# Optimization experiments

Measured on AMD Instinct MI355X. Metric: run time of the kernel, lower is better.

The kernel has to match this reference:

```python
import jax, jax.numpy as jnp
import numpy as np

B, L, D = 2, 2048, 1024
H = 16          # num_heads == num_key_value_heads
FD = 16         # feature_dim (q/k head dim)
HD = D // H     # head_dim = 64 (v head dim)
EPS = 1e-5


def setup_inputs() -> dict:
    key = jax.random.key(0)
    k0, k1, k2, k3, k4 = jax.random.split(key, 5)
    scale = 0.02
    return {
        "hidden_states": jax.random.normal(k0, (B, L, D), jnp.float32),
        "Wq": jax.random.normal(k1, (D, H * FD), jnp.float32) * scale,
        "Wk": jax.random.normal(k2, (D, H * FD), jnp.float32) * scale,
        "Wv": jax.random.normal(k3, (D, H * HD), jnp.float32) * scale,
        "Wo": jax.random.normal(k4, (H * HD, D), jnp.float32) * scale,
    }


def reference(hidden_states, Wq, Wk, Wv, Wo):
    # projections (bias-free), split heads: b l (h d) -> b h l d
    q = (hidden_states @ Wq).reshape(B, L, H, FD).transpose(0, 2, 1, 3)
    k = (hidden_states @ Wk).reshape(B, L, H, FD).transpose(0, 2, 1, 3)
    v = (hidden_states @ Wv).reshape(B, L, H, HD).transpose(0, 2, 1, 3)

    # parallel_rebased: squared-dot-product kernel attention, causal,
    # row-normalized by the kernel sum (use_scale=True, use_normalize=True)
    qk_scale = FD ** -0.5
    s = jnp.einsum('bhqd,bhkd->bhqk', q * qk_scale, k)
    s = s * s  # quadratic feature map: (q.k)^2
    causal = jnp.tril(jnp.ones((L, L), dtype=bool))
    s = jnp.where(causal, s, 0.0)
    z = jnp.sum(s, axis=-1)  # [B,H,L]
    o = jnp.einsum('bhqk,bhkd->bhqd', s, v) / (z[..., None] + EPS)

    # merge heads: b h l d -> b l (h d), output projection
    o = o.transpose(0, 2, 1, 3).reshape(B, L, H * HD)
    return o @ Wo
```

## Files before the change

kernel.cpp:

```cpp
#include <hip/hip_runtime.h>
#include <hip/hip_bf16.h>

#define BB 2
#define LL 2048
#define DD 1024
#define HH 16
#define FD 16
#define HD 64
#define EPS 1e-5f
#define RQKV 1536
#define NFIX 4

typedef __attribute__((ext_vector_type(4))) float f32x4;
typedef __attribute__((ext_vector_type(8))) _Float16 f16x8;
typedef __attribute__((ext_vector_type(4))) _Float16 f16x4;

__global__ __launch_bounds__(256) void cast_hs(
    const float* __restrict__ src, _Float16* __restrict__ dst, int n) {
  int idx = (blockIdx.x * 256 + threadIdx.x) * 16;
  if (idx >= n) return;
#pragma unroll
  for (int half = 0; half < 2; half++) {
    float4 a = *(const float4*)(src + idx + half * 8);
    float4 b = *(const float4*)(src + idx + half * 8 + 4);
    f16x8 p = {(_Float16)a.x, (_Float16)a.y, (_Float16)a.z, (_Float16)a.w,
               (_Float16)b.x, (_Float16)b.y, (_Float16)b.z, (_Float16)b.w};
    *(f16x8*)(dst + idx + half * 8) = p;
  }
}

__global__ __launch_bounds__(256) void transpose_qkv(
    const float* __restrict__ Wq, const float* __restrict__ Wk,
    const float* __restrict__ Wv, _Float16* __restrict__ dst) {
  __shared__ _Float16 s[32][40];
  const int ct = blockIdx.x % 48, kt = blockIdx.x / 48;
  const float* src;
  int n0, ncol, drow;
  if (ct < 8) { src = Wq; n0 = ct * 32; ncol = 256; drow = n0; }
  else if (ct < 16) { src = Wk; n0 = (ct - 8) * 32; ncol = 256; drow = 256 + n0; }
  else { src = Wv; n0 = (ct - 16) * 32; ncol = 1024; drow = 512 + n0; }
  const int k0 = kt * 32;
  const int tid = threadIdx.x;
  {
    int r = tid >> 3, c = (tid & 7) * 4;
    float4 v = *(const float4*)(src + (size_t)(k0 + r) * ncol + n0 + c);
    f16x4 p = {(_Float16)v.x, (_Float16)v.y, (_Float16)v.z, (_Float16)v.w};
    *(f16x4*)&s[r][c] = p;
  }
  __syncthreads();
  {
    int n = tid >> 3, kk = (tid & 7) * 4;
    f16x4 o = {s[kk + 0][n], s[kk + 1][n], s[kk + 2][n], s[kk + 3][n]};
    *(f16x4*)(dst + (size_t)(drow + n) * DD + k0 + kk) = o;
  }
}

__global__ __launch_bounds__(256) void transpose_cast(
    const float* __restrict__ src, _Float16* __restrict__ dst, int K, int N) {
  __shared__ _Float16 s[32][40];
  const int n0 = blockIdx.x * 32, k0 = blockIdx.y * 32;
  const int tid = threadIdx.x;
  {
    int r = tid >> 3, c = (tid & 7) * 4;
    float4 v = *(const float4*)(src + (size_t)(k0 + r) * N + n0 + c);
    f16x4 p = {(_Float16)v.x, (_Float16)v.y, (_Float16)v.z, (_Float16)v.w};
    *(f16x4*)&s[r][c] = p;
  }
  __syncthreads();
  {
    int n = tid >> 3, kk = (tid & 7) * 4;
    f16x4 o = {s[kk + 0][n], s[kk + 1][n], s[kk + 2][n], s[kk + 3][n]};
    *(f16x4*)(dst + (size_t)(n0 + n) * K + k0 + kk) = o;
  }
}

template <typename OutT>
__global__ __launch_bounds__(256) void gemm_f16(
    const _Float16* __restrict__ A, const _Float16* __restrict__ Bt,
    OutT* __restrict__ C, int M, int N, int K) {
  __shared__ __attribute__((aligned(16))) _Float16 sA[128 * 64];
  __shared__ __attribute__((aligned(16))) _Float16 sB[64 * 64];
  const int tid = threadIdx.x;
  const int m0 = blockIdx.y * 128, n0 = blockIdx.x * 64;
  const int w = tid >> 6, lane = tid & 63, quad = lane >> 4, l16 = lane & 15;
  const int wm = (w >> 1) * 64, wn = (w & 1) * 32;

  const int sr = tid >> 1, p = tid & 1;
  const int brow = (tid & 127) >> 1;
  const _Float16* Ag = A + (size_t)(m0 + sr) * K + p * 32;
  const _Float16* Bg = Bt + (size_t)(n0 + brow) * K + p * 32;
  _Float16* sAw = &sA[sr * 64];
  _Float16* sBw = &sB[brow * 64];
  const int aswz = sr & 7, bswz = brow & 7;

  f32x4 acc[4][2];
#pragma unroll
  for (int i = 0; i < 4; i++)
#pragma unroll
    for (int j = 0; j < 2; j++) acc[i][j] = (f32x4){0.f, 0.f, 0.f, 0.f};

  f16x8 ar[4], br[4];
  auto LOAD = [&](int k0) {
#pragma unroll
    for (int i = 0; i < 4; i++) ar[i] = *(const f16x8*)(Ag + k0 + i * 8);
    if (tid < 128) {
#pragma unroll
      for (int i = 0; i < 4; i++) br[i] = *(const f16x8*)(Bg + k0 + i * 8);
    }
  };
  LOAD(0);

  int aoff[4], boff[2];
#pragma unroll
  for (int i = 0; i < 4; i++) {
    int row = wm + i * 16 + l16;
    aoff[i] = row * 64 + ((quad ^ (row & 7)) * 8);
  }
#pragma unroll
  for (int j = 0; j < 2; j++) {
    int row = wn + j * 16 + l16;
    boff[j] = row * 64 + ((quad ^ (row & 7)) * 8);
  }

  for (int k0 = 0; k0 < K; k0 += 64) {
    __syncthreads();
#pragma unroll
    for (int i = 0; i < 4; i++)
      *(f16x8*)(sAw + (((4 * p + i) ^ aswz) * 8)) = ar[i];
    if (tid < 128) {
#pragma unroll
      for (int i = 0; i < 4; i++)
        *(f16x8*)(sBw + (((4 * p + i) ^ bswz) * 8)) = br[i];
    }
    __syncthreads();
    if (k0 + 64 < K) LOAD(k0 + 64);

#pragma unroll
    for (int s = 0; s < 2; s++) {
      f16x8 af[4], bf[2];
#pragma unroll
      for (int i = 0; i < 4; i++) {
        int row = wm + i * 16 + l16;
        int col = ((s * 4 + quad) ^ (row & 7)) * 8;
        af[i] = *(const f16x8*)&sA[row * 64 + col];
      }
#pragma unroll
      for (int j = 0; j < 2; j++) {
        int row = wn + j * 16 + l16;
        int col = ((s * 4 + quad) ^ (row & 7)) * 8;
        bf[j] = *(const f16x8*)&sB[row * 64 + col];
      }
#pragma unroll
      for (int i = 0; i < 4; i++)
#pragma unroll
        for (int j = 0; j < 2; j++)
          acc[i][j] = __builtin_amdgcn_mfma_f32_16x16x32_f16(af[i], bf[j], acc[i][j], 0, 0, 0);
    }
  }
  (void)aoff; (void)boff;

#pragma unroll
  for (int i = 0; i < 4; i++)
#pragma unroll
    for (int j = 0; j < 2; j++)
#pragma unroll
      for (int r = 0; r < 4; r++) {
        const int row = m0 + wm + i * 16 + quad * 4 + r;
        const int col = n0 + wn + j * 16 + l16;
        C[(size_t)row * N + col] = (OutT)acc[i][j][r];
      }
}

#define SK4 24
#define SV4 88
#define SS4 88

__global__ __launch_bounds__(256) void attn_mfma4(
    const _Float16* __restrict__ QKV, _Float16* __restrict__ O) {
  __shared__ __attribute__((aligned(16))) _Float16 sK[64 * SK4];
  __shared__ __attribute__((aligned(16))) _Float16 sVt[80 * SV4];
  __shared__ __attribute__((aligned(16))) _Float16 sS2[4 * 32 * SS4];

  const int bh = blockIdx.y;
  const int b = bh >> 4, h = bh & 15;
  const int qtA = blockIdx.x;
  const int qtB = 31 - qtA;
  const int tid = threadIdx.x;
  const int w = tid >> 6;
  const int lane = tid & 63;
  const int quad = lane >> 4;
  const int l16 = lane & 15;
  const int gqA = qtA * 64 + w * 16;
  const int gqB = qtB * 64 + w * 16;

  f16x8 qfragA = {}, qfragB = {};
  if (quad < 2) {
    qfragA = *(const f16x8*)(QKV +
        (size_t)(b * LL + gqA + l16) * RQKV + h * FD + quad * 8);
    qfragB = *(const f16x8*)(QKV +
        (size_t)(b * LL + gqB + l16) * RQKV + h * FD + quad * 8);
  }

  for (int t = tid; t < 16 * SV4; t += 256) {
    int r = t / SV4, c = t % SV4;
    sVt[64 * SV4 + t] = (_Float16)((r == 0 && c < 64) ? 1.0f : 0.0f);
  }
  __syncthreads();
  const f16x8 zf0 = *(const f16x8*)&sVt[(64 + l16) * SV4 + quad * 8];
  const f16x8 zf1 = *(const f16x8*)&sVt[(64 + l16) * SV4 + 32 + quad * 8];

  f32x4 oaccA[4], oaccB[4];
  f32x4 zaccA = (f32x4){0.f, 0.f, 0.f, 0.f};
  f32x4 zaccB = (f32x4){0.f, 0.f, 0.f, 0.f};
#pragma unroll
  for (int nt = 0; nt < 4; nt++) {
    oaccA[nt] = (f32x4){0.f, 0.f, 0.f, 0.f};
    oaccB[nt] = (f32x4){0.f, 0.f, 0.f, 0.f};
  }

  _Float16* sS2B = sS2 + w * 32 * SS4;
  _Float16* sS2A = sS2B + 16 * SS4;

  const int ktiles = qtB + 1;

  const int skey = tid >> 2, sfg = (tid & 3) * 4;
  uint2 kreg;
  f16x8 vreg0, vreg1;
  auto LOAD = [&](int kt) {
    kreg = *(const uint2*)(QKV +
        (size_t)(b * LL + kt * 64 + skey) * RQKV + 256 + h * FD + sfg);
    const _Float16* vp = QKV +
        (size_t)(b * LL + kt * 64 + lane) * RQKV + 512 + h * HD + w * 16;
    vreg0 = *(const f16x8*)vp;
    vreg1 = *(const f16x8*)(vp + 8);
  };
  LOAD(0);

  for (int kt = 0; kt < ktiles; kt++) {
    __syncthreads();
    *(uint2*)&sK[skey * SK4 + sfg] = kreg;
#pragma unroll
    for (int t = 0; t < 8; t++) sVt[(w * 16 + t) * SV4 + lane] = vreg0[t];
#pragma unroll
    for (int t = 0; t < 8; t++) sVt[(w * 16 + 8 + t) * SV4 + lane] = vreg1[t];
    __syncthreads();
    if (kt + 1 < ktiles) LOAD(kt + 1);

    const int k0 = kt * 64;
    const bool activeA = (kt <= qtA);

    f16x8 kf[4];
#pragma unroll
    for (int nt = 0; nt < 4; nt++) {
      f16x8 f = {};
      if (quad < 2) f = *(const f16x8*)&sK[(nt * 16 + l16) * SK4 + quad * 8];
      kf[nt] = f;
    }

    {
      const bool mask = (kt == qtB);
#pragma unroll
      for (int nt = 0; nt < 4; nt++) {
        f32x4 s = __builtin_amdgcn_mfma_f32_16x16x32_f16(
            qfragB, kf[nt], (f32x4){0.f, 0.f, 0.f, 0.f}, 0, 0, 0);
        const int gk = k0 + nt * 16 + l16;
#pragma unroll
        for (int r = 0; r < 4; r++) {
          float sv = s[r] * s[r] * 2.0f;
          if (mask) sv = (gk <= gqB + quad * 4 + r) ? sv : 0.0f;
          sS2B[(quad * 4 + r) * SS4 + nt * 16 + l16] = (_Float16)sv;
        }
      }
    }
    if (activeA) {
      const bool mask = (kt == qtA);
#pragma unroll
      for (int nt = 0; nt < 4; nt++) {
        f32x4 s = __builtin_amdgcn_mfma_f32_16x16x32_f16(
            qfragA, kf[nt], (f32x4){0.f, 0.f, 0.f, 0.f}, 0, 0, 0);
        const int gk = k0 + nt * 16 + l16;
#pragma unroll
        for (int r = 0; r < 4; r++) {
          float sv = s[r] * s[r] * 2.0f;
          if (mask) sv = (gk <= gqA + quad * 4 + r) ? sv : 0.0f;
          sS2A[(quad * 4 + r) * SS4 + nt * 16 + l16] = (_Float16)sv;
        }
      }
    }
    __asm__ volatile("s_waitcnt lgkmcnt(0)" ::: "memory");

    f16x8 afB0 = *(const f16x8*)&sS2B[l16 * SS4 + quad * 8];
    f16x8 afB1 = *(const f16x8*)&sS2B[l16 * SS4 + 32 + quad * 8];
    f16x8 afA0 = {}, afA1 = {};
    if (activeA) {
      afA0 = *(const f16x8*)&sS2A[l16 * SS4 + quad * 8];
      afA1 = *(const f16x8*)&sS2A[l16 * SS4 + 32 + quad * 8];
    }

#pragma unroll
    for (int nt = 0; nt < 4; nt++) {
      f16x8 vf0 = *(const f16x8*)&sVt[(nt * 16 + l16) * SV4 + quad * 8];
      f16x8 vf1 = *(const f16x8*)&sVt[(nt * 16 + l16) * SV4 + 32 + quad * 8];
      oaccB[nt] = __builtin_amdgcn_mfma_f32_16x16x32_f16(afB0, vf0, oaccB[nt], 0, 0, 0);
      oaccB[nt] = __builtin_amdgcn_mfma_f32_16x16x32_f16(afB1, vf1, oaccB[nt], 0, 0, 0);
      if (activeA) {
        oaccA[nt] = __builtin_amdgcn_mfma_f32_16x16x32_f16(afA0, vf0, oaccA[nt], 0, 0, 0);
        oaccA[nt] = __builtin_amdgcn_mfma_f32_16x16x32_f16(afA1, vf1, oaccA[nt], 0, 0, 0);
      }
    }
    zaccB = __builtin_amdgcn_mfma_f32_16x16x32_f16(afB0, zf0, zaccB, 0, 0, 0);
    zaccB = __builtin_amdgcn_mfma_f32_16x16x32_f16(afB1, zf1, zaccB, 0, 0, 0);
    if (activeA) {
      zaccA = __builtin_amdgcn_mfma_f32_16x16x32_f16(afA0, zf0, zaccA, 0, 0, 0);
      zaccA = __builtin_amdgcn_mfma_f32_16x16x32_f16(afA1, zf1, zaccA, 0, 0, 0);
    }
  }

  {
    float rz[4];
#pragma unroll
    for (int r = 0; r < 4; r++) {
      float zz = __shfl(zaccB[r], lane & 48);
      rz[r] = 1.0f / (zz + 32.0f * EPS);
    }
#pragma unroll
    for (int nt = 0; nt < 4; nt++)
#pragma unroll
      for (int r = 0; r < 4; r++) {
        const int gq = gqB + quad * 4 + r;
        O[(size_t)(b * LL + gq) * (HH * HD) + h * HD + nt * 16 + l16] =
            (_Float16)(oaccB[nt][r] * rz[r]);
      }
  }
  {
    float rz[4];
#pragma unroll
    for (int r = 0; r < 4; r++) {
      float zz = __shfl(zaccA[r], lane & 48);
      rz[r] = 1.0f / (zz + 32.0f * EPS);
    }
#pragma unroll
    for (int nt = 0; nt < 4; nt++)
#pragma unroll
      for (int r = 0; r < 4; r++) {
        const int gq = gqA + quad * 4 + r;
        O[(size_t)(b * LL + gq) * (HH * HD) + h * HD + nt * 16 + l16] =
            (_Float16)(oaccA[nt][r] * rz[r]);
      }
  }
}

__global__ __launch_bounds__(256) void early_qkv(
    const float* __restrict__ hs, const float* __restrict__ Wq,
    const float* __restrict__ Wk, const float* __restrict__ Wv,
    float* __restrict__ QKVe) {
  __shared__ float sHS[8][DD];
  __shared__ float part[8][8][32];
  const int tid = threadIdx.x;
  const int kg = tid >> 5, c = tid & 31;
  const int c0 = blockIdx.x * 32;

  for (int i = tid; i < 8 * (DD / 4); i += 256) {
    int e = i / (DD / 4), col4 = (i % (DD / 4)) * 4;
    int b = e >> 2, r = e & 3;
    *(float4*)&sHS[e][col4] =
        *(const float4*)(hs + (size_t)(b * LL + r) * DD + col4);
  }
  __syncthreads();

  const float* W;
  int col, ncol;
  if (c0 < 256) { W = Wq; col = c0 + c; ncol = 256; }
  else if (c0 < 512) { W = Wk; col = (c0 - 256) + c; ncol = 256; }
  else { W = Wv; col = (c0 - 512) + c; ncol = 1024; }

  float acc[8] = {};
  const int d0 = kg * 128;
#pragma unroll 4
  for (int d = d0; d < d0 + 128; d++) {
    float wv = W[(size_t)d * ncol + col];
#pragma unroll
    for (int e = 0; e < 8; e++) acc[e] += sHS[e][d] * wv;
  }
#pragma unroll
  for (int e = 0; e < 8; e++) part[kg][e][c] = acc[e];
  __syncthreads();

  {
    int e = tid >> 5;
    float t = 0.f;
#pragma unroll
    for (int g = 0; g < 8; g++) t += part[g][e][c];
    QKVe[(size_t)e * RQKV + c0 + c] = t;
  }
}

__global__ __launch_bounds__(256) void fix_final(
    const float* __restrict__ QKVe, _Float16* __restrict__ Oatt) {
  const int b = blockIdx.x >> 4, h = blockIdx.x & 15;
  const int tid = threadIdx.x;
  const int p = tid >> 6, d = tid & 63;

  float num = 0.f, z = 0.f;
  const float* qrow = QKVe + (size_t)(b * 4 + p) * RQKV + h * FD;
  for (int j = 0; j <= p; j++) {
    const float* krow = QKVe + (size_t)(b * 4 + j) * RQKV + 256 + h * FD;
    float s = 0.f;
#pragma unroll
    for (int f = 0; f < FD; f++) s += qrow[f] * krow[f];
    s *= 0.25f;
    s = s * s;
    z += s;
    num += s * QKVe[(size_t)(b * 4 + j) * RQKV + 512 + h * HD + d];
  }
  Oatt[(size_t)(b * LL + p) * (HH * HD) + h * HD + d] =
      (_Float16)(num / (z + EPS));
}

extern "C" void kernel_launch(void* const* d_in, const int* in_sizes, int n_in,
                              void* d_out, int out_size, void* d_ws, size_t ws_size,
                              hipStream_t stream) {
  const float* hs = (const float*)d_in[0];
  const float* Wq = (const float*)d_in[1];
  const float* Wk = (const float*)d_in[2];
  const float* Wv = (const float*)d_in[3];
  const float* Wo = (const float*)d_in[4];
  float* out = (float*)d_out;

  char* ws = (char*)d_ws;
  _Float16* WqkvT = (_Float16*)ws;
  _Float16* WoT   = (_Float16*)(ws + (3ull << 20));
  _Float16* HS16  = (_Float16*)(ws + (5ull << 20));
  _Float16* QKV   = (_Float16*)(ws + (13ull << 20));
  _Float16* Oatt  = (_Float16*)(ws + (25ull << 20));
  float*    QKVe  = (float*)(ws + (33ull << 20));

  const int M = BB * LL;

  cast_hs<<<dim3(M * DD / (256 * 16)), 256, 0, stream>>>(hs, HS16, M * DD);
  transpose_qkv<<<dim3(48 * 32), 256, 0, stream>>>(Wq, Wk, Wv, WqkvT);
  transpose_cast<<<dim3(DD / 32, DD / 32), 256, 0, stream>>>(Wo, WoT, DD, DD);

  early_qkv<<<dim3(RQKV / 32), 256, 0, stream>>>(hs, Wq, Wk, Wv, QKVe);

  gemm_f16<_Float16><<<dim3(RQKV / 64, M / 128), 256, 0, stream>>>(
      HS16, WqkvT, QKV, M, RQKV, DD);

  attn_mfma4<<<dim3(LL / 128, BB * HH), 256, 0, stream>>>(QKV, Oatt);

  fix_final<<<dim3(BB * HH), 256, 0, stream>>>(QKVe, Oatt);

  gemm_f16<float><<<dim3(DD / 64, M / 128), 256, 0, stream>>>(
      Oatt, WoT, out, M, DD, DD);
}
```

Baseline: 175.5 us.

## Fuse prep kernels, cast activations inside QKV GEMM, fold fixup into attention

Merges the two weight transpose kernels and the early QKV projection into one launch. It drops the separate fp16 cast of hidden_states by having the QKV GEMM load fp32 rows and convert them while writing shared memory. It also folds the first-rows fixup into an extra block column of the attention kernel, with predicated stores so the two writers do not collide. This cuts launches and one full activation round-trip, at the cost of larger fp32 global loads in the GEMM and a race-free but ordering-sensitive split of row writes.

New measurement: 208.0 us. 1.19x slower.

```diff
diff --git a/kernel.cpp b/kernel.cpp
--- a/kernel.cpp
+++ b/kernel.cpp
@@ -15,68 +15,90 @@
 typedef __attribute__((ext_vector_type(8))) _Float16 f16x8;
 typedef __attribute__((ext_vector_type(4))) _Float16 f16x4;
 
-__global__ __launch_bounds__(256) void cast_hs(
-    const float* __restrict__ src, _Float16* __restrict__ dst, int n) {
-  int idx = (blockIdx.x * 256 + threadIdx.x) * 16;
-  if (idx >= n) return;
-#pragma unroll
-  for (int half = 0; half < 2; half++) {
-    float4 a = *(const float4*)(src + idx + half * 8);
-    float4 b = *(const float4*)(src + idx + half * 8 + 4);
-    f16x8 p = {(_Float16)a.x, (_Float16)a.y, (_Float16)a.z, (_Float16)a.w,
-               (_Float16)b.x, (_Float16)b.y, (_Float16)b.z, (_Float16)b.w};
-    *(f16x8*)(dst + idx + half * 8) = p;
+__global__ __launch_bounds__(256) void prep(
+    const float* __restrict__ Wq, const float* __restrict__ Wk,
+    const float* __restrict__ Wv, const float* __restrict__ Wo,
+    const float* __restrict__ hs, _Float16* __restrict__ WqkvT,
+    _Float16* __restrict__ WoT, float* __restrict__ QKVe) {
+  __shared__ __attribute__((aligned(16))) char smem[40960];
+  const int bx = blockIdx.x;
+  const int tid = threadIdx.x;
+
+  if (bx < 2560) {
+    _Float16(*s)[40] = (_Float16(*)[40])smem;
+    const float* src;
+    _Float16* dst;
+    int n0, ncol, drow, k0;
+    if (bx < 1536) {
+      int ct = bx % 48, kt = bx / 48;
+      if (ct < 8) { src = Wq; n0 = ct * 32; ncol = 256; drow = n0; }
+      else if (ct < 16) { src = Wk; n0 = (ct - 8) * 32; ncol = 256; drow = 256 + n0; }
+      else { src = Wv; n0 = (ct - 16) * 32; ncol = 1024; drow = 512 + n0; }
+      k0 = kt * 32;
+      dst = WqkvT;
+    } else {
+      int i2 = bx - 1536;
+      n0 = (i2 & 31) * 32; k0 = (i2 >> 5) * 32;
+      src = Wo; ncol = DD; drow = n0; dst = WoT;
+    }
+    {
+      int r = tid >> 3, c = (tid & 7) * 4;
+      float4 v = *(const float4*)(src + (size_t)(k0 + r) * ncol + n0 + c);
+      f16x4 p = {(_Float16)v.x, (_Float16)v.y, (_Float16)v.z, (_Float16)v.w};
+      *(f16x4*)&s[r][c] = p;
+    }
+    __syncthreads();
+    {
+      int n = tid >> 3, kk = (tid & 7) * 4;
+      f16x4 o = {s[kk + 0][n], s[kk + 1][n], s[kk + 2][n], s[kk + 3][n]};
+      *(f16x4*)(dst + (size_t)(drow + n) * DD + k0 + kk) = o;
+    }
+    return;
+  }
+
+  float(*sHS)[DD] = (float(*)[DD])smem;
+  float(*part)[8][32] = (float(*)[8][32])(smem + 32768);
+  const int kg = tid >> 5, c = tid & 31;
+  const int c0 = (bx - 2560) * 32;
+
+  for (int i = tid; i < 8 * (DD / 4); i += 256) {
+    int e = i / (DD / 4), col4 = (i % (DD / 4)) * 4;
+    int b = e >> 2, r = e & 3;
+    *(float4*)&sHS[e][col4] =
+        *(const float4*)(hs + (size_t)(b * LL + r) * DD + col4);
+  }
+  __syncthreads();
+
+  const float* W;
+  int col, ncol;
+  if (c0 < 256) { W = Wq; col = c0 + c; ncol = 256; }
+  else if (c0 < 512) { W = Wk; col = (c0 - 256) + c; ncol = 256; }
+  else { W = Wv; col = (c0 - 512) + c; ncol = 1024; }
+
+  float acc[8] = {};
+  const int d0 = kg * 128;
+#pragma unroll 4
+  for (int d = d0; d < d0 + 128; d++) {
+    float wv = W[(size_t)d * ncol + col];
+#pragma unroll
+    for (int e = 0; e < 8; e++) acc[e] += sHS[e][d] * wv;
+  }
+#pragma unroll
+  for (int e = 0; e < 8; e++) part[kg][e][c] = acc[e];
+  __syncthreads();
+
+  {
+    int e = tid >> 5;
+    float t = 0.f;
+#pragma unroll
+    for (int g = 0; g < 8; g++) t += part[g][e][c];
+    QKVe[(size_t)e * RQKV + c0 + c] = t;
   }
 }
 
-__global__ __launch_bounds__(256) void transpose_qkv(
-    const float* __restrict__ Wq, const float* __restrict__ Wk,
-    const float* __restrict__ Wv, _Float16* __restrict__ dst) {
-  __shared__ _Float16 s[32][40];
-  const int ct = blockIdx.x % 48, kt = blockIdx.x / 48;
-  const float* src;
-  int n0, ncol, drow;
-  if (ct < 8) { src = Wq; n0 = ct * 32; ncol = 256; drow = n0; }
-  else if (ct < 16) { src = Wk; n0 = (ct - 8) * 32; ncol = 256; drow = 256 + n0; }
-  else { src = Wv; n0 = (ct - 16) * 32; ncol = 1024; drow = 512 + n0; }
-  const int k0 = kt * 32;
-  const int tid = threadIdx.x;
-  {
-    int r = tid >> 3, c = (tid & 7) * 4;
-    float4 v = *(const float4*)(src + (size_t)(k0 + r) * ncol + n0 + c);
-    f16x4 p = {(_Float16)v.x, (_Float16)v.y, (_Float16)v.z, (_Float16)v.w};
-    *(f16x4*)&s[r][c] = p;
-  }
-  __syncthreads();
-  {
-    int n = tid >> 3, kk = (tid & 7) * 4;
-    f16x4 o = {s[kk + 0][n], s[kk + 1][n], s[kk + 2][n], s[kk + 3][n]};
-    *(f16x4*)(dst + (size_t)(drow + n) * DD + k0 + kk) = o;
-  }
-}
-
-__global__ __launch_bounds__(256) void transpose_cast(
-    const float* __restrict__ src, _Float16* __restrict__ dst, int K, int N) {
-  __shared__ _Float16 s[32][40];
-  const int n0 = blockIdx.x * 32, k0 = blockIdx.y * 32;
-  const int tid = threadIdx.x;
-  {
-    int r = tid >> 3, c = (tid & 7) * 4;
-    float4 v = *(const float4*)(src + (size_t)(k0 + r) * N + n0 + c);
-    f16x4 p = {(_Float16)v.x, (_Float16)v.y, (_Float16)v.z, (_Float16)v.w};
-    *(f16x4*)&s[r][c] = p;
-  }
-  __syncthreads();
-  {
-    int n = tid >> 3, kk = (tid & 7) * 4;
-    f16x4 o = {s[kk + 0][n], s[kk + 1][n], s[kk + 2][n], s[kk + 3][n]};
-    *(f16x4*)(dst + (size_t)(n0 + n) * K + k0 + kk) = o;
-  }
-}
-
-template <typename OutT>
+template <typename AT, typename OutT>
 __global__ __launch_bounds__(256) void gemm_f16(
-    const _Float16* __restrict__ A, const _Float16* __restrict__ Bt,
+    const AT* __restrict__ A, const _Float16* __restrict__ Bt,
     OutT* __restrict__ C, int M, int N, int K) {
   __shared__ __attribute__((aligned(16))) _Float16 sA[128 * 64];
   __shared__ __attribute__((aligned(16))) _Float16 sB[64 * 64];
@@ -87,7 +109,7 @@
 
   const int sr = tid >> 1, p = tid & 1;
   const int brow = (tid & 127) >> 1;
-  const _Float16* Ag = A + (size_t)(m0 + sr) * K + p * 32;
+  const AT* Ag = A + (size_t)(m0 + sr) * K + p * 32;
   const _Float16* Bg = Bt + (size_t)(n0 + brow) * K + p * 32;
   _Float16* sAw = &sA[sr * 64];
   _Float16* sBw = &sB[brow * 64];
@@ -99,10 +121,17 @@
 #pragma unroll
     for (int j = 0; j < 2; j++) acc[i][j] = (f32x4){0.f, 0.f, 0.f, 0.f};
 
-  f16x8 ar[4], br[4];
+  f16x8 ar[4];
+  float4 ar32[8];
+  f16x8 br[4];
   auto LOAD = [&](int k0) {
-#pragma unroll
-    for (int i = 0; i < 4; i++) ar[i] = *(const f16x8*)(Ag + k0 + i * 8);
+    if constexpr (sizeof(AT) == 4) {
+#pragma unroll
+      for (int i = 0; i < 8; i++) ar32[i] = *(const float4*)(Ag + k0 + i * 4);
+    } else {
+#pragma unroll
+      for (int i = 0; i < 4; i++) ar[i] = *(const f16x8*)(Ag + k0 + i * 8);
+    }
     if (tid < 128) {
 #pragma unroll
       for (int i = 0; i < 4; i++) br[i] = *(const f16x8*)(Bg + k0 + i * 8);
@@ -110,23 +139,21 @@
   };
   LOAD(0);
 
-  int aoff[4], boff[2];
-#pragma unroll
-  for (int i = 0; i < 4; i++) {
-    int row = wm + i * 16 + l16;
-    aoff[i] = row * 64 + ((quad ^ (row & 7)) * 8);
-  }
-#pragma unroll
-  for (int j = 0; j < 2; j++) {
-    int row = wn + j * 16 + l16;
-    boff[j] = row * 64 + ((quad ^ (row & 7)) * 8);
-  }
-
   for (int k0 = 0; k0 < K; k0 += 64) {
     __syncthreads();
-#pragma unroll
-    for (int i = 0; i < 4; i++)
-      *(f16x8*)(sAw + (((4 * p + i) ^ aswz) * 8)) = ar[i];
+    if constexpr (sizeof(AT) == 4) {
+#pragma unroll
+      for (int i = 0; i < 4; i++) {
+        float4 lo = ar32[2 * i], hi = ar32[2 * i + 1];
+        f16x8 pk = {(_Float16)lo.x, (_Float16)lo.y, (_Float16)lo.z, (_Float16)lo.w,
+                    (_Float16)hi.x, (_Float16)hi.y, (_Float16)hi.z, (_Float16)hi.w};
+        *(f16x8*)(sAw + (((4 * p + i) ^ aswz) * 8)) = pk;
+      }
+    } else {
+#pragma unroll
+      for (int i = 0; i < 4; i++)
+        *(f16x8*)(sAw + (((4 * p + i) ^ aswz) * 8)) = ar[i];
+    }
     if (tid < 128) {
 #pragma unroll
       for (int i = 0; i < 4; i++)
@@ -157,7 +184,6 @@
           acc[i][j] = __builtin_amdgcn_mfma_f32_16x16x32_f16(af[i], bf[j], acc[i][j], 0, 0, 0);
     }
   }
-  (void)aoff; (void)boff;
 
 #pragma unroll
   for (int i = 0; i < 4; i++)
@@ -175,17 +201,38 @@
 #define SV4 88
 #define SS4 88
 
-__global__ __launch_bounds__(256) void attn_mfma4(
-    const _Float16* __restrict__ QKV, _Float16* __restrict__ O) {
+__global__ __launch_bounds__(256) void attn_mfma5(
+    const _Float16* __restrict__ QKV, const float* __restrict__ QKVe,
+    _Float16* __restrict__ O) {
+  const int bh = blockIdx.y;
+  const int b = bh >> 4, h = bh & 15;
+  const int tid = threadIdx.x;
+
+  if (blockIdx.x == 16) {
+    const int p = tid >> 6, d = tid & 63;
+    float num = 0.f, z = 0.f;
+    const float* qrow = QKVe + (size_t)(b * 4 + p) * RQKV + h * FD;
+    for (int j = 0; j <= p; j++) {
+      const float* krow = QKVe + (size_t)(b * 4 + j) * RQKV + 256 + h * FD;
+      float s = 0.f;
+#pragma unroll
+      for (int f = 0; f < FD; f++) s += qrow[f] * krow[f];
+      s *= 0.25f;
+      s = s * s;
+      z += s;
+      num += s * QKVe[(size_t)(b * 4 + j) * RQKV + 512 + h * HD + d];
+    }
+    O[(size_t)(b * LL + p) * (HH * HD) + h * HD + d] =
+        (_Float16)(num / (z + EPS));
+    return;
+  }
+
   __shared__ __attribute__((aligned(16))) _Float16 sK[64 * SK4];
   __shared__ __attribute__((aligned(16))) _Float16 sVt[80 * SV4];
   __shared__ __attribute__((aligned(16))) _Float16 sS2[4 * 32 * SS4];
 
-  const int bh = blockIdx.y;
-  const int b = bh >> 4, h = bh & 15;
   const int qtA = blockIdx.x;
   const int qtB = 31 - qtA;
-  const int tid = threadIdx.x;
   const int w = tid >> 6;
   const int lane = tid & 63;
   const int quad = lane >> 4;
@@ -344,77 +391,11 @@
 #pragma unroll
       for (int r = 0; r < 4; r++) {
         const int gq = gqA + quad * 4 + r;
-        O[(size_t)(b * LL + gq) * (HH * HD) + h * HD + nt * 16 + l16] =
-            (_Float16)(oaccA[nt][r] * rz[r]);
-      }
-  }
-}
-
-__global__ __launch_bounds__(256) void early_qkv(
-    const float* __restrict__ hs, const float* __restrict__ Wq,
-    const float* __restrict__ Wk, const float* __restrict__ Wv,
-    float* __restrict__ QKVe) {
-  __shared__ float sHS[8][DD];
-  __shared__ float part[8][8][32];
-  const int tid = threadIdx.x;
-  const int kg = tid >> 5, c = tid & 31;
-  const int c0 = blockIdx.x * 32;
-
-  for (int i = tid; i < 8 * (DD / 4); i += 256) {
-    int e = i / (DD / 4), col4 = (i % (DD / 4)) * 4;
-    int b = e >> 2, r = e & 3;
-    *(float4*)&sHS[e][col4] =
-        *(const float4*)(hs + (size_t)(b * LL + r) * DD + col4);
-  }
-  __syncthreads();
-
-  const float* W;
-  int col, ncol;
-  if (c0 < 256) { W = Wq; col = c0 + c; ncol = 256; }
-  else if (c0 < 512) { W = Wk; col = (c0 - 256) + c; ncol = 256; }
-  else { W = Wv; col = (c0 - 512) + c; ncol = 1024; }
-
-  float acc[8] = {};
-  const int d0 = kg * 128;
-#pragma unroll 4
-  for (int d = d0; d < d0 + 128; d++) {
-    float wv = W[(size_t)d * ncol + col];
-#pragma unroll
-    for (int e = 0; e < 8; e++) acc[e] += sHS[e][d] * wv;
-  }
-#pragma unroll
-  for (int e = 0; e < 8; e++) part[kg][e][c] = acc[e];
-  __syncthreads();
-
-  {
-    int e = tid >> 5;
-    float t = 0.f;
-#pragma unroll
-    for (int g = 0; g < 8; g++) t += part[g][e][c];
-    QKVe[(size_t)e * RQKV + c0 + c] = t;
-  }
-}
-
-__global__ __launch_bounds__(256) void fix_final(
-    const float* __restrict__ QKVe, _Float16* __restrict__ Oatt) {
-  const int b = blockIdx.x >> 4, h = blockIdx.x & 15;
-  const int tid = threadIdx.x;
-  const int p = tid >> 6, d = tid & 63;
-
-  float num = 0.f, z = 0.f;
-  const float* qrow = QKVe + (size_t)(b * 4 + p) * RQKV + h * FD;
-  for (int j = 0; j <= p; j++) {
-    const float* krow = QKVe + (size_t)(b * 4 + j) * RQKV + 256 + h * FD;
-    float s = 0.f;
-#pragma unroll
-    for (int f = 0; f < FD; f++) s += qrow[f] * krow[f];
-    s *= 0.25f;
-    s = s * s;
-    z += s;
-    num += s * QKVe[(size_t)(b * 4 + j) * RQKV + 512 + h * HD + d];
-  }
-  Oatt[(size_t)(b * LL + p) * (HH * HD) + h * HD + d] =
-      (_Float16)(num / (z + EPS));
+        if (gq >= NFIX || qtA != 0)
+          O[(size_t)(b * LL + gq) * (HH * HD) + h * HD + nt * 16 + l16] =
+              (_Float16)(oaccA[nt][r] * rz[r]);
+      }
+  }
 }
 
 extern "C" void kernel_launch(void* const* d_in, const int* in_sizes, int n_in,
@@ -430,26 +411,19 @@
   char* ws = (char*)d_ws;
   _Float16* WqkvT = (_Float16*)ws;
   _Float16* WoT   = (_Float16*)(ws + (3ull << 20));
-  _Float16* HS16  = (_Float16*)(ws + (5ull << 20));
-  _Float16* QKV   = (_Float16*)(ws + (13ull << 20));
-  _Float16* Oatt  = (_Float16*)(ws + (25ull << 20));
-  float*    QKVe  = (float*)(ws + (33ull << 20));
+  _Float16* QKV   = (_Float16*)(ws + (5ull << 20));
+  _Float16* Oatt  = (_Float16*)(ws + (17ull << 20));
+  float*    QKVe  = (float*)(ws + (25ull << 20));
 
   const int M = BB * LL;
 
-  cast_hs<<<dim3(M * DD / (256 * 16)), 256, 0, stream>>>(hs, HS16, M * DD);
-  transpose_qkv<<<dim3(48 * 32), 256, 0, stream>>>(Wq, Wk, Wv, WqkvT);
-  transpose_cast<<<dim3(DD / 32, DD / 32), 256, 0, stream>>>(Wo, WoT, DD, DD);
-
-  early_qkv<<<dim3(RQKV / 32), 256, 0, stream>>>(hs, Wq, Wk, Wv, QKVe);
-
-  gemm_f16<_Float16><<<dim3(RQKV / 64, M / 128), 256, 0, stream>>>(
-      HS16, WqkvT, QKV, M, RQKV, DD);
-
-  attn_mfma4<<<dim3(LL / 128, BB * HH), 256, 0, stream>>>(QKV, Oatt);
-
-  fix_final<<<dim3(BB * HH), 256, 0, stream>>>(QKVe, Oatt);
-
-  gemm_f16<float><<<dim3(DD / 64, M / 128), 256, 0, stream>>>(
+  prep<<<dim3(2608), 256, 0, stream>>>(Wq, Wk, Wv, Wo, hs, WqkvT, WoT, QKVe);
+
+  gemm_f16<float, _Float16><<<dim3(RQKV / 64, M / 128), 256, 0, stream>>>(
+      hs, WqkvT, QKV, M, RQKV, DD);
+
+  attn_mfma5<<<dim3(17, BB * HH), 256, 0, stream>>>(QKV, QKVe, Oatt);
+
+  gemm_f16<_Float16, float><<<dim3(DD / 64, M / 128), 256, 0, stream>>>(
       Oatt, WoT, out, M, DD, DD);
 }
```
